# Kernel tuning notes

Measured on AMD Instinct MI355X. Metric: run time of the kernel, lower is better.

Reference implementation:

```python
import jax, jax.numpy as jnp
import numpy as np

# ---- module geometry ----
BULK = 64          # bulk (J2) integration points, 3 comps each
COH = 32           # cohesive integration points, 2 comps each
LS = BULK * 3 + COH * 2  # = 256, material layer width

# ---- J2 plasticity material constants (plane-stress, linear isotropic hardening) ----
E_MOD = 200.0
NU = 0.3
SY0 = 2.0
HARD = 10.0
G_MOD = E_MOD / (2.0 * (1.0 + NU))
_c = E_MOD / (1.0 - NU * NU)
C_EL = np.array([[_c, _c * NU, 0.0], [_c * NU, _c, 0.0], [0.0, 0.0, _c * (1.0 - NU) / 2.0]], dtype=np.float32)
C_INV = np.linalg.inv(C_EL).astype(np.float32)

# ---- Turon cohesive-zone constants (bilinear damage law) ----
K_PEN = 50.0       # penalty stiffness
DELTA0 = 0.1       # damage-onset effective jump
DELTAF = 1.0       # full-failure effective jump


def j2_update(eps, epsp, epbar):
    # eps, epsp: [B,P,3]; epbar: [B,P]. Radial-return with linear hardening.
    sig_tr = jnp.einsum('bpi,ji->bpj', eps - epsp, jnp.asarray(C_EL))
    s1, s2, s12 = sig_tr[..., 0], sig_tr[..., 1], sig_tr[..., 2]
    seq = jnp.sqrt(jnp.maximum(s1 * s1 - s1 * s2 + s2 * s2 + 3.0 * s12 * s12, 1e-12))
    f = seq - (SY0 + HARD * epbar)
    plastic = f > 0.0
    dep = jnp.where(plastic, f / (3.0 * G_MOD + HARD), 0.0)
    r = (SY0 + HARD * (epbar + dep)) / seq
    sig = jnp.where(plastic[..., None], r[..., None] * sig_tr, sig_tr)
    epsp_new = jnp.where(plastic[..., None], eps - jnp.einsum('bpj,ij->bpi', sig, jnp.asarray(C_INV)), epsp)
    return sig, epsp_new, epbar + dep


def coh_update(jump, hist):
    # jump: [B,P,2] (normal, shear); hist: [B,P] max effective jump (damage history).
    dn, ds = jump[..., 0], jump[..., 1]
    lam = jnp.sqrt(jnp.maximum(jnp.maximum(dn, 0.0) ** 2 + ds * ds, 1e-12))
    hist_new = jnp.maximum(hist, lam)
    dmg = jnp.clip(DELTAF * (hist_new - DELTA0) / (jnp.maximum(hist_new, 1e-12) * (DELTAF - DELTA0)), 0.0, 1.0)
    tn = K_PEN * dn * jnp.where(dn > 0.0, 1.0 - dmg, 1.0)  # compression is undamaged
    ts = (1.0 - dmg) * K_PEN * ds
    return jnp.stack([tn, ts], axis=-1), hist_new


def setup_inputs() -> dict:
    key = jax.random.key(0)
    k1, k2, k3 = jax.random.split(key, 3)
    x = jax.random.normal(k1, (256, 1024, 16), dtype=jnp.float32)
    W1 = jax.random.normal(k2, (LS, 16), dtype=jnp.float32) * 0.1
    W2 = jax.random.normal(k3, (16, LS), dtype=jnp.float32) * 0.1
    return {"x": x, "W1": W1, "W2": W2}


def reference(x, W1, W2):
    B, T, F = x.shape
    # fc1 applied to every (batch, time) slice (original loops; here one GEMM)
    h = jnp.einsum('btf,lf->btl', x, W1)  # [B,T,LS]
    h_t = jnp.transpose(h, (1, 0, 2))     # [T,B,LS] for the time scan

    epsp0 = jnp.zeros((B, BULK, 3), dtype=x.dtype)
    epbar0 = jnp.zeros((B, BULK), dtype=x.dtype)
    hist0 = jnp.zeros((B, COH), dtype=x.dtype)

    def step(carry, ht):
        epsp, epbar, hist = carry
        eps = ht[:, : BULK * 3].reshape(B, BULK, 3)
        jmp = ht[:, BULK * 3:].reshape(B, COH, 2)
        sig, epsp, epbar = j2_update(eps, epsp, epbar)   # update + commit per step
        trac, hist = coh_update(jmp, hist)
        y = jnp.concatenate([sig.reshape(B, -1), trac.reshape(B, -1)], axis=-1)
        return (epsp, epbar, hist), y

    _, ys = jax.lax.scan(step, (epsp0, epbar0, hist0), h_t)  # [T,B,LS]
    ys = jnp.transpose(ys, (1, 0, 2))  # [B,T,LS]
    # softLayer fc2: linear with softplus-constrained (non-negative) weights
    out = jnp.einsum('btl,ol->bto', ys, jax.nn.softplus(W2))
    return out
```

## Files before the change

### kernel.cpp

```cpp
#include <hip/hip_runtime.h>
#include <cmath>
#include <cstdint>

#define BATCH  256
#define TT     1024
#define FIN    16
#define LSZ    256
#define NBULK  64
#define NCOH   32
#define TC     32
#define NCHUNK (TT / TC)
#define HBS    260
#define HCS    68
#define YSS    336

typedef __attribute__((ext_vector_type(8))) short short8;
typedef __attribute__((ext_vector_type(4))) float floatx4;

__device__ __forceinline__ unsigned short f2bf_rne(float f) {
    union { float f; unsigned int i; } v; v.f = f;
    unsigned int b = v.i;
    return (unsigned short)((b + 0x7FFFu + ((b >> 16) & 1u)) >> 16);
}
__device__ __forceinline__ unsigned int bfbits(float f) {
    union { float f; unsigned int i; } v; v.f = f;
    return v.i + 0x8000u;
}
__device__ __forceinline__ float u2f(unsigned int u) {
    union { unsigned int i; float f; } v; v.i = u; return v.f;
}

#define BARRIER() asm volatile("s_waitcnt lgkmcnt(0)\n\ts_barrier" ::: "memory")

#define MC00   219.78021978021977f
#define MC01   65.93406593406593f
#define MC22   76.92307692307692f
#define MSY0   2.0f
#define AK     0.958466453674121406f
#define BK     0.041533546325878594f

__global__ __launch_bounds__(256, 1)
void fused_mat_kernel(const float* __restrict__ x,
                      const float* __restrict__ w1,
                      const float* __restrict__ w2,
                      float* __restrict__ out)
{
    __shared__ __attribute__((aligned(16))) float          s_hb[2][TC][HBS];
    __shared__ __attribute__((aligned(16))) float          s_hc[2][TC][HCS];
    __shared__ __attribute__((aligned(16))) unsigned short s_y [2][TC][YSS];

    const int tid  = threadIdx.x;
    const int b    = blockIdx.x;
    const int lane = tid & 63;
    const int wv   = tid >> 6;
    const int m    = lane & 15;
    const int q    = lane >> 4;

    const size_t xrow = (size_t)b * TT;

    short8 w1fd[12];
    short8 w1f4[4];
    short8 vf[10];
    uint4  rxc[2][2], rxp[2][2];

    if (wv == 2) {
        #pragma unroll
        for (int n = 0; n < 12; ++n) {
            #pragma unroll
            for (int j = 0; j < 8; ++j) {
                float v = 0.f;
                if (q < 2) {
                    const int l = n * 16 + m, c = l / 3, cm = l - 3 * c, f = q * 8 + j;
                    const float wa = w1[(3 * c + 0) * FIN + f];
                    const float wb = w1[(3 * c + 1) * FIN + f];
                    const float wc = w1[(3 * c + 2) * FIN + f];
                    v = (cm == 0) ? fmaf(MC01, wb, MC00 * wa)
                      : (cm == 1) ? fmaf(MC00, wb, MC01 * wa)
                                  : MC22 * wc;
                }
                w1fd[n][j] = (short)f2bf_rne(v);
            }
        }
        #pragma unroll
        for (int n = 12; n < 16; ++n) {
            #pragma unroll
            for (int j = 0; j < 8; ++j) {
                unsigned short v = 0;
                if (q < 2) v = f2bf_rne(w1[(n * 16 + m) * FIN + q * 8 + j]);
                w1f4[n - 12][j] = (short)v;
            }
        }
        #pragma unroll
        for (int mt = 0; mt < 2; ++mt) {
            short8 ax, adx;
            #pragma unroll
            for (int j = 0; j < 8; ++j) {
                float xc = 0.f, xp = 0.f;
                if (q < 2) {
                    const int rowB = mt * 16 + m;
                    xc = x[(xrow + rowB) * FIN + q * 8 + j];
                    if (rowB > 0) xp = x[(xrow + rowB - 1) * FIN + q * 8 + j];
                }
                ax[j]  = (short)f2bf_rne(xc);
                adx[j] = (short)f2bf_rne(xc - xp);
            }
            #pragma unroll
            for (int n = 0; n < 16; ++n) {
                floatx4 acc = {0.f, 0.f, 0.f, 0.f};
                acc = (n < 12)
                    ? __builtin_amdgcn_mfma_f32_16x16x32_bf16(adx, w1fd[n], acc, 0, 0, 0)
                    : __builtin_amdgcn_mfma_f32_16x16x32_bf16(ax, w1f4[n - 12], acc, 0, 0, 0);
                const int col = n * 16 + m;
                if (n < 12) {
                    const int cc = col / 3, cm = col - cc * 3;
                    #pragma unroll
                    for (int r = 0; r < 4; ++r)
                        s_hb[0][mt * 16 + q * 4 + r][cc * 4 + cm] = acc[r];
                } else {
                    #pragma unroll
                    for (int r = 0; r < 4; ++r)
                        s_hc[0][mt * 16 + q * 4 + r][col - 192] = acc[r];
                }
            }
        }
        if (q < 2) {
            #pragma unroll
            for (int mt = 0; mt < 2; ++mt) {
                const int rowB = TC + mt * 16 + m;
                const float* xc = x + (xrow + rowB) * FIN + q * 8;
                const float* xp = x + (xrow + rowB - 1) * FIN + q * 8;
                rxc[mt][0] = *(const uint4*)xc;  rxc[mt][1] = *(const uint4*)(xc + 4);
                rxp[mt][0] = *(const uint4*)xp;  rxp[mt][1] = *(const uint4*)(xp + 4);
            }
        }
    } else if (wv == 3) {
        #pragma unroll
        for (int ks = 0; ks < 10; ++ks) {
            #pragma unroll
            for (int j = 0; j < 8; ++j) {
                const int p = ks * 32 + q * 8 + j;
                unsigned short v = 0;
                if (p < 256) {
                    const int comp = p & 3;
                    if (comp < 3) {
                        const int l = 3 * (p >> 2) + comp;
                        float xv = w2[m * LSZ + l];
                        float sp = fmaxf(xv, 0.0f) + log1pf(expf(-fabsf(xv)));
                        v = f2bf_rne(sp);
                    }
                } else {
                    const int l = p - 64;
                    float xv = w2[m * LSZ + l];
                    float sp = fmaxf(xv, 0.0f) + log1pf(expf(-fabsf(xv)));
                    v = f2bf_rne(sp);
                }
                vf[ks][j] = (short)v;
            }
        }
    }

    float sg0 = 0.f, sg1 = 0.f, sg2 = 0.f, syv = MSY0;
    float hist = 0.f;

    __syncthreads();

    for (int i = 0; i <= NCHUNK; ++i) {
        if (wv == 0) {
            if (i < NCHUNK) {
                const float* hb = &s_hb[i & 1][0][0];
                unsigned short* yb = &s_y[i & 1][0][0];
                const int off = lane * 4;
                #pragma unroll
                for (int t = 0; t < TC; ++t) {
                    const floatx4 dv = *(const floatx4*)(hb + t * HBS + off);
                    const float pre = AK * syv;
                    const float t0 = sg0 + dv.x, t1 = sg1 + dv.y, t2 = sg2 + dv.z;
                    const float a1 = t0 * (t0 - t1);
                    const float b1 = fmaf(t1, t1, 3.0f * (t2 * t2));
                    const float qq = fmaxf(a1 + b1, 1e-12f);
                    const float rs  = __builtin_amdgcn_rsqf(qq);
                    const float seq = qq * rs;
                    const float rr  = fminf(fmaf(pre, rs, BK), 1.0f);
                    sg0 = rr * t0; sg1 = rr * t1; sg2 = rr * t2;
                    syv = fmaf(BK, fmaxf(seq - syv, 0.0f), syv);
                    uint2 pk;
                    pk.x = (bfbits(sg0) >> 16) | (bfbits(sg1) & 0xFFFF0000u);
                    pk.y = (bfbits(sg2) >> 16);
                    *(uint2*)(yb + t * YSS + off) = pk;
                }
            }
        } else if (wv == 1) {
            if (i < NCHUNK && lane < NCOH) {
                const float* hc = &s_hc[i & 1][0][0];
                unsigned short* yb = &s_y[i & 1][0][0];
                const int off = 2 * lane;
                #pragma unroll
                for (int t = 0; t < TC; ++t) {
                    const float2 jv = *(const float2*)(hc + t * HCS + off);
                    const float dn = jv.x, ds = jv.y;
                    const float dnp = fmaxf(dn, 0.0f);
                    const float lam = __builtin_amdgcn_sqrtf(fmaxf(fmaf(dnp, dnp, ds * ds), 1e-12f));
                    hist = fmaxf(hist, lam);
                    float dmg = (hist - 0.1f) * __builtin_amdgcn_rcpf(hist * 0.9f);
                    dmg = fminf(fmaxf(dmg, 0.0f), 1.0f);
                    const float om = 1.0f - dmg;
                    const float tn = 50.0f * dn * (dn > 0.0f ? om : 1.0f);
                    const float ts = om * 50.0f * ds;
                    unsigned int pk = (bfbits(tn) >> 16) | (bfbits(ts) & 0xFFFF0000u);
                    *(unsigned int*)(yb + t * YSS + 256 + off) = pk;
                }
            }
        } else if (wv == 2) {
            if (i + 1 < NCHUNK) {
                short8 ax[2], adx[2];
                #pragma unroll
                for (int mt = 0; mt < 2; ++mt) {
                    const unsigned int wc[8] = {rxc[mt][0].x, rxc[mt][0].y, rxc[mt][0].z, rxc[mt][0].w,
                                                rxc[mt][1].x, rxc[mt][1].y, rxc[mt][1].z, rxc[mt][1].w};
                    const unsigned int wp[8] = {rxp[mt][0].x, rxp[mt][0].y, rxp[mt][0].z, rxp[mt][0].w,
                                                rxp[mt][1].x, rxp[mt][1].y, rxp[mt][1].z, rxp[mt][1].w};
                    #pragma unroll
                    for (int j = 0; j < 8; ++j) {
                        unsigned short va = 0, vd = 0;
                        if (q < 2) {
                            const float xc = u2f(wc[j]), xp = u2f(wp[j]);
                            va = f2bf_rne(xc);
                            vd = f2bf_rne(xc - xp);
                        }
                        ax[mt][j]  = (short)va;
                        adx[mt][j] = (short)vd;
                    }
                }
                if (i + 2 < NCHUNK && q < 2) {
                    #pragma unroll
                    for (int mt = 0; mt < 2; ++mt) {
                        const int rowB = (i + 2) * TC + mt * 16 + m;
                        const float* xc = x + (xrow + rowB) * FIN + q * 8;
                        const float* xp = x + (xrow + rowB - 1) * FIN + q * 8;
                        rxc[mt][0] = *(const uint4*)xc;  rxc[mt][1] = *(const uint4*)(xc + 4);
                        rxp[mt][0] = *(const uint4*)xp;  rxp[mt][1] = *(const uint4*)(xp + 4);
                    }
                }
                float* hbw = &s_hb[(i + 1) & 1][0][0];
                float* hcw = &s_hc[(i + 1) & 1][0][0];
                #pragma unroll
                for (int mt = 0; mt < 2; ++mt) {
                    #pragma unroll
                    for (int n = 0; n < 16; ++n) {
                        floatx4 acc = {0.f, 0.f, 0.f, 0.f};
                        acc = (n < 12)
                            ? __builtin_amdgcn_mfma_f32_16x16x32_bf16(adx[mt], w1fd[n], acc, 0, 0, 0)
                            : __builtin_amdgcn_mfma_f32_16x16x32_bf16(ax[mt], w1f4[n - 12], acc, 0, 0, 0);
                        const int col = n * 16 + m;
                        if (n < 12) {
                            const int cc = col / 3, cm = col - cc * 3;
                            #pragma unroll
                            for (int r = 0; r < 4; ++r)
                                hbw[(mt * 16 + q * 4 + r) * HBS + cc * 4 + cm] = acc[r];
                        } else {
                            #pragma unroll
                            for (int r = 0; r < 4; ++r)
                                hcw[(mt * 16 + q * 4 + r) * HCS + col - 192] = acc[r];
                        }
                    }
                }
            }
        } else {
            if (i >= 1) {
                const int t0 = (i - 1) * TC;
                const unsigned short* yb = &s_y[(i - 1) & 1][0][0];
                #pragma unroll
                for (int mt = 0; mt < 2; ++mt) {
                    floatx4 a0 = {0.f, 0.f, 0.f, 0.f};
                    floatx4 a1 = {0.f, 0.f, 0.f, 0.f};
                    #pragma unroll
                    for (int ks = 0; ks < 5; ++ks) {
                        const short8* yp = (const short8*)(yb + (mt * 16 + m) * YSS + ks * 32 + q * 8);
                        a0 = __builtin_amdgcn_mfma_f32_16x16x32_bf16(*yp, vf[ks], a0, 0, 0, 0);
                    }
                    #pragma unroll
                    for (int ks = 5; ks < 10; ++ks) {
                        const short8* yp = (const short8*)(yb + (mt * 16 + m) * YSS + ks * 32 + q * 8);
                        a1 = __builtin_amdgcn_mfma_f32_16x16x32_bf16(*yp, vf[ks], a1, 0, 0, 0);
                    }
                    #pragma unroll
                    for (int r = 0; r < 4; ++r)
                        out[(xrow + t0 + mt * 16 + q * 4 + r) * FIN + m] = a0[r] + a1[r];
                }
            }
        }
        BARRIER();
    }
}

extern "C" void kernel_launch(void* const* d_in, const int* in_sizes, int n_in,
                              void* d_out, int out_size, void* d_ws, size_t ws_size,
                              hipStream_t stream) {
    const float* x  = (const float*)d_in[0];
    const float* w1 = (const float*)d_in[1];
    const float* w2 = (const float*)d_in[2];
    float* out = (float*)d_out;
    fused_mat_kernel<<<BATCH, 256, 0, stream>>>(x, w1, w2, out);
}
```

Before: 160.6 us.

## Split bulk GEMM into bf16 hi/lo terms and batch LDS loads in recurrence waves

The bulk-strain GEMM path now splits the increment inputs and the folded W1 weights into bf16 high and low parts. It issues three MFMAs per tile instead of one, which recovers near-fp32 accuracy for the accumulated stress trial. The J2 and cohesive recurrence waves now prefetch eight timesteps of LDS inputs into registers, double-buffered behind scheduling barriers, so the serial per-step chain does not wait on individual LDS loads. The cost is triple the MFMA work in the producer wave and more register pressure.

```diff
diff --git a/kernel.cpp b/kernel.cpp
--- a/kernel.cpp
+++ b/kernel.cpp
@@ -29,6 +29,11 @@
 __device__ __forceinline__ float u2f(unsigned int u) {
     union { unsigned int i; float f; } v; v.i = u; return v.f;
 }
+__device__ __forceinline__ void bfsplit(float v, unsigned short& hi, unsigned short& lo) {
+    unsigned short h = f2bf_rne(v);
+    lo = f2bf_rne(v - u2f((unsigned int)h << 16));
+    hi = h;
+}
 
 #define BARRIER() asm volatile("s_waitcnt lgkmcnt(0)\n\ts_barrier" ::: "memory")
 
@@ -58,7 +63,7 @@
 
     const size_t xrow = (size_t)b * TT;
 
-    short8 w1fd[12];
+    short8 w1fdh[12], w1fdl[12];
     short8 w1f4[4];
     short8 vf[10];
     uint4  rxc[2][2], rxp[2][2];
@@ -78,7 +83,10 @@
                       : (cm == 1) ? fmaf(MC00, wb, MC01 * wa)
                                   : MC22 * wc;
                 }
-                w1fd[n][j] = (short)f2bf_rne(v);
+                unsigned short hi, lo;
+                bfsplit(v, hi, lo);
+                w1fdh[n][j] = (short)hi;
+                w1fdl[n][j] = (short)lo;
             }
         }
         #pragma unroll
@@ -92,7 +100,7 @@
         }
         #pragma unroll
         for (int mt = 0; mt < 2; ++mt) {
-            short8 ax, adx;
+            short8 ax, adh, adl;
             #pragma unroll
             for (int j = 0; j < 8; ++j) {
                 float xc = 0.f, xp = 0.f;
@@ -101,15 +109,22 @@
                     xc = x[(xrow + rowB) * FIN + q * 8 + j];
                     if (rowB > 0) xp = x[(xrow + rowB - 1) * FIN + q * 8 + j];
                 }
+                unsigned short hi, lo;
+                bfsplit(xc - xp, hi, lo);
                 ax[j]  = (short)f2bf_rne(xc);
-                adx[j] = (short)f2bf_rne(xc - xp);
+                adh[j] = (short)hi;
+                adl[j] = (short)lo;
             }
             #pragma unroll
             for (int n = 0; n < 16; ++n) {
                 floatx4 acc = {0.f, 0.f, 0.f, 0.f};
-                acc = (n < 12)
-                    ? __builtin_amdgcn_mfma_f32_16x16x32_bf16(adx, w1fd[n], acc, 0, 0, 0)
-                    : __builtin_amdgcn_mfma_f32_16x16x32_bf16(ax, w1f4[n - 12], acc, 0, 0, 0);
+                if (n < 12) {
+                    acc = __builtin_amdgcn_mfma_f32_16x16x32_bf16(adh, w1fdh[n], acc, 0, 0, 0);
+                    acc = __builtin_amdgcn_mfma_f32_16x16x32_bf16(adl, w1fdh[n], acc, 0, 0, 0);
+                    acc = __builtin_amdgcn_mfma_f32_16x16x32_bf16(adh, w1fdl[n], acc, 0, 0, 0);
+                } else {
+                    acc = __builtin_amdgcn_mfma_f32_16x16x32_bf16(ax, w1f4[n - 12], acc, 0, 0, 0);
+                }
                 const int col = n * 16 + m;
                 if (n < 12) {
                     const int cc = col / 3, cm = col - cc * 3;
@@ -170,23 +185,39 @@
                 const float* hb = &s_hb[i & 1][0][0];
                 unsigned short* yb = &s_y[i & 1][0][0];
                 const int off = lane * 4;
-                #pragma unroll
-                for (int t = 0; t < TC; ++t) {
-                    const floatx4 dv = *(const floatx4*)(hb + t * HBS + off);
-                    const float pre = AK * syv;
-                    const float t0 = sg0 + dv.x, t1 = sg1 + dv.y, t2 = sg2 + dv.z;
-                    const float a1 = t0 * (t0 - t1);
-                    const float b1 = fmaf(t1, t1, 3.0f * (t2 * t2));
-                    const float qq = fmaxf(a1 + b1, 1e-12f);
-                    const float rs  = __builtin_amdgcn_rsqf(qq);
-                    const float seq = qq * rs;
-                    const float rr  = fminf(fmaf(pre, rs, BK), 1.0f);
-                    sg0 = rr * t0; sg1 = rr * t1; sg2 = rr * t2;
-                    syv = fmaf(BK, fmaxf(seq - syv, 0.0f), syv);
-                    uint2 pk;
-                    pk.x = (bfbits(sg0) >> 16) | (bfbits(sg1) & 0xFFFF0000u);
-                    pk.y = (bfbits(sg2) >> 16);
-                    *(uint2*)(yb + t * YSS + off) = pk;
+                floatx4 ev[2][8];
+                #pragma unroll
+                for (int t = 0; t < 8; ++t)
+                    ev[0][t] = *(const floatx4*)(hb + t * HBS + off);
+                __builtin_amdgcn_sched_barrier(0);
+                #pragma unroll
+                for (int g = 0; g < 4; ++g) {
+                    if (g + 1 < 4) {
+                        #pragma unroll
+                        for (int t = 0; t < 8; ++t)
+                            ev[(g + 1) & 1][t] =
+                                *(const floatx4*)(hb + ((g + 1) * 8 + t) * HBS + off);
+                        __builtin_amdgcn_sched_barrier(0);
+                    }
+                    #pragma unroll
+                    for (int tt = 0; tt < 8; ++tt) {
+                        const int t = g * 8 + tt;
+                        const floatx4 dv = ev[g & 1][tt];
+                        const float pre = AK * syv;
+                        const float t0 = sg0 + dv.x, t1 = sg1 + dv.y, t2 = sg2 + dv.z;
+                        const float a1 = t0 * (t0 - t1);
+                        const float b1 = fmaf(t1, t1, 3.0f * (t2 * t2));
+                        const float qq = fmaxf(a1 + b1, 1e-12f);
+                        const float rs  = __builtin_amdgcn_rsqf(qq);
+                        const float seq = qq * rs;
+                        const float rr  = fminf(fmaf(pre, rs, BK), 1.0f);
+                        sg0 = rr * t0; sg1 = rr * t1; sg2 = rr * t2;
+                        syv = fmaf(BK, fmaxf(seq - syv, 0.0f), syv);
+                        uint2 pk;
+                        pk.x = (bfbits(sg0) >> 16) | (bfbits(sg1) & 0xFFFF0000u);
+                        pk.y = (bfbits(sg2) >> 16);
+                        *(uint2*)(yb + t * YSS + off) = pk;
+                    }
                 }
             }
         } else if (wv == 1) {
@@ -194,25 +225,40 @@
                 const float* hc = &s_hc[i & 1][0][0];
                 unsigned short* yb = &s_y[i & 1][0][0];
                 const int off = 2 * lane;
-                #pragma unroll
-                for (int t = 0; t < TC; ++t) {
-                    const float2 jv = *(const float2*)(hc + t * HCS + off);
-                    const float dn = jv.x, ds = jv.y;
-                    const float dnp = fmaxf(dn, 0.0f);
-                    const float lam = __builtin_amdgcn_sqrtf(fmaxf(fmaf(dnp, dnp, ds * ds), 1e-12f));
-                    hist = fmaxf(hist, lam);
-                    float dmg = (hist - 0.1f) * __builtin_amdgcn_rcpf(hist * 0.9f);
-                    dmg = fminf(fmaxf(dmg, 0.0f), 1.0f);
-                    const float om = 1.0f - dmg;
-                    const float tn = 50.0f * dn * (dn > 0.0f ? om : 1.0f);
-                    const float ts = om * 50.0f * ds;
-                    unsigned int pk = (bfbits(tn) >> 16) | (bfbits(ts) & 0xFFFF0000u);
-                    *(unsigned int*)(yb + t * YSS + 256 + off) = pk;
+                float2 jv[2][8];
+                #pragma unroll
+                for (int t = 0; t < 8; ++t)
+                    jv[0][t] = *(const float2*)(hc + t * HCS + off);
+                __builtin_amdgcn_sched_barrier(0);
+                #pragma unroll
+                for (int g = 0; g < 4; ++g) {
+                    if (g + 1 < 4) {
+                        #pragma unroll
+                        for (int t = 0; t < 8; ++t)
+                            jv[(g + 1) & 1][t] =
+                                *(const float2*)(hc + ((g + 1) * 8 + t) * HCS + off);
+                        __builtin_amdgcn_sched_barrier(0);
+                    }
+                    #pragma unroll
+                    for (int tt = 0; tt < 8; ++tt) {
+                        const int t = g * 8 + tt;
+                        const float dn = jv[g & 1][tt].x, ds = jv[g & 1][tt].y;
+                        const float dnp = fmaxf(dn, 0.0f);
+                        const float lam = __builtin_amdgcn_sqrtf(fmaxf(fmaf(dnp, dnp, ds * ds), 1e-12f));
+                        hist = fmaxf(hist, lam);
+                        float dmg = (hist - 0.1f) * __builtin_amdgcn_rcpf(hist * 0.9f);
+                        dmg = fminf(fmaxf(dmg, 0.0f), 1.0f);
+                        const float om = 1.0f - dmg;
+                        const float tn = 50.0f * dn * (dn > 0.0f ? om : 1.0f);
+                        const float ts = om * 50.0f * ds;
+                        unsigned int pk = (bfbits(tn) >> 16) | (bfbits(ts) & 0xFFFF0000u);
+                        *(unsigned int*)(yb + t * YSS + 256 + off) = pk;
+                    }
                 }
             }
         } else if (wv == 2) {
             if (i + 1 < NCHUNK) {
-                short8 ax[2], adx[2];
+                short8 ax[2], adh[2], adl[2];
                 #pragma unroll
                 for (int mt = 0; mt < 2; ++mt) {
                     const unsigned int wc[8] = {rxc[mt][0].x, rxc[mt][0].y, rxc[mt][0].z, rxc[mt][0].w,
@@ -221,14 +267,15 @@
                                                 rxp[mt][1].x, rxp[mt][1].y, rxp[mt][1].z, rxp[mt][1].w};
                     #pragma unroll
                     for (int j = 0; j < 8; ++j) {
-                        unsigned short va = 0, vd = 0;
+                        unsigned short va = 0, vh = 0, vl = 0;
                         if (q < 2) {
                             const float xc = u2f(wc[j]), xp = u2f(wp[j]);
                             va = f2bf_rne(xc);
-                            vd = f2bf_rne(xc - xp);
+                            bfsplit(xc - xp, vh, vl);
                         }
                         ax[mt][j]  = (short)va;
-                        adx[mt][j] = (short)vd;
+                        adh[mt][j] = (short)vh;
+                        adl[mt][j] = (short)vl;
                     }
                 }
                 if (i + 2 < NCHUNK && q < 2) {
@@ -248,9 +295,13 @@
                     #pragma unroll
                     for (int n = 0; n < 16; ++n) {
                         floatx4 acc = {0.f, 0.f, 0.f, 0.f};
-                        acc = (n < 12)
-                            ? __builtin_amdgcn_mfma_f32_16x16x32_bf16(adx[mt], w1fd[n], acc, 0, 0, 0)
-                            : __builtin_amdgcn_mfma_f32_16x16x32_bf16(ax[mt], w1f4[n - 12], acc, 0, 0, 0);
+                        if (n < 12) {
+                            acc = __builtin_amdgcn_mfma_f32_16x16x32_bf16(adh[mt], w1fdh[n], acc, 0, 0, 0);
+                            acc = __builtin_amdgcn_mfma_f32_16x16x32_bf16(adl[mt], w1fdh[n], acc, 0, 0, 0);
+                            acc = __builtin_amdgcn_mfma_f32_16x16x32_bf16(adh[mt], w1fdl[n], acc, 0, 0, 0);
+                        } else {
+                            acc = __builtin_amdgcn_mfma_f32_16x16x32_bf16(ax[mt], w1f4[n - 12], acc, 0, 0, 0);
+                        }
                         const int col = n * 16 + m;
                         if (n < 12) {
                             const int cc = col / 3, cm = col - cc * 3;
```

Measured after the change: 163.3 us. Within noise of the previous version (+1.7%).

## Rotate J2 stress basis, split-bf16 fc1, halve chunk size, move bf16 packing to fc2

Applied to the files above, without the earlier changes.

Rewrites the J2 recurrence in a rotated (u,v,w) stress basis so the equivalent-stress form is diagonal. The basis change and the cohesive penalty scale are folded into the W1 and softplus(W2) fragments. The fc1 bulk GEMM now uses a hi/lo bf16 split (three MFMAs) for better accuracy. The time chunk shrinks from 32 to 16 steps, which shortens the pipeline fill and drain but doubles the number of barriers. Material outputs are stored to LDS as fp32, and the fc2 wave converts them to bf16, taking packing work off the serial recurrence waves at the cost of more LDS traffic.

```diff
diff --git a/kernel.cpp b/kernel.cpp
--- a/kernel.cpp
+++ b/kernel.cpp
@@ -6,13 +6,12 @@
 #define TT     1024
 #define FIN    16
 #define LSZ    256
-#define NBULK  64
 #define NCOH   32
-#define TC     32
+#define TC     16
 #define NCHUNK (TT / TC)
 #define HBS    260
 #define HCS    68
-#define YSS    336
+#define YFS    324
 
 typedef __attribute__((ext_vector_type(8))) short short8;
 typedef __attribute__((ext_vector_type(4))) float floatx4;
@@ -22,18 +21,23 @@
     unsigned int b = v.i;
     return (unsigned short)((b + 0x7FFFu + ((b >> 16) & 1u)) >> 16);
 }
-__device__ __forceinline__ unsigned int bfbits(float f) {
+__device__ __forceinline__ unsigned short f2bf_hu(float f) {
     union { float f; unsigned int i; } v; v.f = f;
-    return v.i + 0x8000u;
+    return (unsigned short)((v.i + 0x8000u) >> 16);
 }
 __device__ __forceinline__ float u2f(unsigned int u) {
     union { unsigned int i; float f; } v; v.i = u; return v.f;
 }
+__device__ __forceinline__ void bfsplit(float v, unsigned short& hi, unsigned short& lo) {
+    unsigned short h = f2bf_rne(v);
+    lo = f2bf_rne(v - u2f((unsigned int)h << 16));
+    hi = h;
+}
 
 #define BARRIER() asm volatile("s_waitcnt lgkmcnt(0)\n\ts_barrier" ::: "memory")
 
-#define MC00   219.78021978021977f
-#define MC01   65.93406593406593f
+#define MCU    285.71428571428571f
+#define MCV    153.84615384615384f
 #define MC22   76.92307692307692f
 #define MSY0   2.0f
 #define AK     0.958466453674121406f
@@ -45,9 +49,9 @@
                       const float* __restrict__ w2,
                       float* __restrict__ out)
 {
-    __shared__ __attribute__((aligned(16))) float          s_hb[2][TC][HBS];
-    __shared__ __attribute__((aligned(16))) float          s_hc[2][TC][HCS];
-    __shared__ __attribute__((aligned(16))) unsigned short s_y [2][TC][YSS];
+    __shared__ __attribute__((aligned(16))) float s_hb[2][TC][HBS];
+    __shared__ __attribute__((aligned(16))) float s_hc[2][TC][HCS];
+    __shared__ __attribute__((aligned(16))) float s_yf[2][TC][YFS];
 
     const int tid  = threadIdx.x;
     const int b    = blockIdx.x;
@@ -58,10 +62,10 @@
 
     const size_t xrow = (size_t)b * TT;
 
-    short8 w1fd[12];
+    short8 w1fdh[12], w1fdl[12];
     short8 w1f4[4];
     short8 vf[10];
-    uint4  rxc[2][2], rxp[2][2];
+    uint4  rxc[2], rxp[2];
 
     if (wv == 2) {
         #pragma unroll
@@ -74,11 +78,14 @@
                     const float wa = w1[(3 * c + 0) * FIN + f];
                     const float wb = w1[(3 * c + 1) * FIN + f];
                     const float wc = w1[(3 * c + 2) * FIN + f];
-                    v = (cm == 0) ? fmaf(MC01, wb, MC00 * wa)
-                      : (cm == 1) ? fmaf(MC00, wb, MC01 * wa)
+                    v = (cm == 0) ? MCU * (wa + wb)
+                      : (cm == 1) ? MCV * (wa - wb)
                                   : MC22 * wc;
                 }
-                w1fd[n][j] = (short)f2bf_rne(v);
+                unsigned short hi, lo;
+                bfsplit(v, hi, lo);
+                w1fdh[n][j] = (short)hi;
+                w1fdl[n][j] = (short)lo;
             }
         }
         #pragma unroll
@@ -90,48 +97,50 @@
                 w1f4[n - 12][j] = (short)v;
             }
         }
-        #pragma unroll
-        for (int mt = 0; mt < 2; ++mt) {
-            short8 ax, adx;
+        {
+            short8 ax, adh, adl;
             #pragma unroll
             for (int j = 0; j < 8; ++j) {
                 float xc = 0.f, xp = 0.f;
                 if (q < 2) {
-                    const int rowB = mt * 16 + m;
-                    xc = x[(xrow + rowB) * FIN + q * 8 + j];
-                    if (rowB > 0) xp = x[(xrow + rowB - 1) * FIN + q * 8 + j];
-                }
+                    xc = x[(xrow + m) * FIN + q * 8 + j];
+                    if (m > 0) xp = x[(xrow + m - 1) * FIN + q * 8 + j];
+                }
+                unsigned short hi, lo;
+                bfsplit(xc - xp, hi, lo);
                 ax[j]  = (short)f2bf_rne(xc);
-                adx[j] = (short)f2bf_rne(xc - xp);
+                adh[j] = (short)hi;
+                adl[j] = (short)lo;
             }
             #pragma unroll
             for (int n = 0; n < 16; ++n) {
                 floatx4 acc = {0.f, 0.f, 0.f, 0.f};
-                acc = (n < 12)
-                    ? __builtin_amdgcn_mfma_f32_16x16x32_bf16(adx, w1fd[n], acc, 0, 0, 0)
-                    : __builtin_amdgcn_mfma_f32_16x16x32_bf16(ax, w1f4[n - 12], acc, 0, 0, 0);
+                if (n < 12) {
+                    acc = __builtin_amdgcn_mfma_f32_16x16x32_bf16(adh, w1fdh[n], acc, 0, 0, 0);
+                    acc = __builtin_amdgcn_mfma_f32_16x16x32_bf16(adl, w1fdh[n], acc, 0, 0, 0);
+                    acc = __builtin_amdgcn_mfma_f32_16x16x32_bf16(adh, w1fdl[n], acc, 0, 0, 0);
+                } else {
+                    acc = __builtin_amdgcn_mfma_f32_16x16x32_bf16(ax, w1f4[n - 12], acc, 0, 0, 0);
+                }
                 const int col = n * 16 + m;
                 if (n < 12) {
                     const int cc = col / 3, cm = col - cc * 3;
                     #pragma unroll
                     for (int r = 0; r < 4; ++r)
-                        s_hb[0][mt * 16 + q * 4 + r][cc * 4 + cm] = acc[r];
+                        s_hb[0][q * 4 + r][cc * 4 + cm] = acc[r];
                 } else {
                     #pragma unroll
                     for (int r = 0; r < 4; ++r)
-                        s_hc[0][mt * 16 + q * 4 + r][col - 192] = acc[r];
+                        s_hc[0][q * 4 + r][col - 192] = acc[r];
                 }
             }
         }
         if (q < 2) {
-            #pragma unroll
-            for (int mt = 0; mt < 2; ++mt) {
-                const int rowB = TC + mt * 16 + m;
-                const float* xc = x + (xrow + rowB) * FIN + q * 8;
-                const float* xp = x + (xrow + rowB - 1) * FIN + q * 8;
-                rxc[mt][0] = *(const uint4*)xc;  rxc[mt][1] = *(const uint4*)(xc + 4);
-                rxp[mt][0] = *(const uint4*)xp;  rxp[mt][1] = *(const uint4*)(xp + 4);
-            }
+            const int rowB = TC + m;
+            const float* xc = x + (xrow + rowB) * FIN + q * 8;
+            const float* xp = x + (xrow + rowB - 1) * FIN + q * 8;
+            rxc[0] = *(const uint4*)xc;  rxc[1] = *(const uint4*)(xc + 4);
+            rxp[0] = *(const uint4*)xp;  rxp[1] = *(const uint4*)(xp + 4);
         }
     } else if (wv == 3) {
         #pragma unroll
@@ -139,27 +148,31 @@
             #pragma unroll
             for (int j = 0; j < 8; ++j) {
                 const int p = ks * 32 + q * 8 + j;
-                unsigned short v = 0;
+                float v = 0.f;
                 if (p < 256) {
                     const int comp = p & 3;
                     if (comp < 3) {
-                        const int l = 3 * (p >> 2) + comp;
-                        float xv = w2[m * LSZ + l];
-                        float sp = fmaxf(xv, 0.0f) + log1pf(expf(-fabsf(xv)));
-                        v = f2bf_rne(sp);
+                        const int c = p >> 2;
+                        const float w0v = w2[m * LSZ + 3 * c + 0];
+                        const float w1v = w2[m * LSZ + 3 * c + 1];
+                        const float w2v = w2[m * LSZ + 3 * c + 2];
+                        const float sp0 = fmaxf(w0v, 0.f) + log1pf(expf(-fabsf(w0v)));
+                        const float sp1 = fmaxf(w1v, 0.f) + log1pf(expf(-fabsf(w1v)));
+                        const float sp2 = fmaxf(w2v, 0.f) + log1pf(expf(-fabsf(w2v)));
+                        v = (comp == 0) ? 0.5f * (sp0 + sp1)
+                          : (comp == 1) ? 0.5f * (sp0 - sp1)
+                                        : sp2;
                     }
                 } else {
-                    const int l = p - 64;
-                    float xv = w2[m * LSZ + l];
-                    float sp = fmaxf(xv, 0.0f) + log1pf(expf(-fabsf(xv)));
-                    v = f2bf_rne(sp);
-                }
-                vf[ks][j] = (short)v;
+                    const float xv = w2[m * LSZ + (p - 64)];
+                    v = 50.0f * (fmaxf(xv, 0.f) + log1pf(expf(-fabsf(xv))));
+                }
+                vf[ks][j] = (short)f2bf_rne(v);
             }
         }
     }
 
-    float sg0 = 0.f, sg1 = 0.f, sg2 = 0.f, syv = MSY0;
+    float sgu = 0.f, sgv = 0.f, sgw = 0.f, syv = MSY0;
     float hist = 0.f;
 
     __syncthreads();
@@ -168,125 +181,128 @@
         if (wv == 0) {
             if (i < NCHUNK) {
                 const float* hb = &s_hb[i & 1][0][0];
-                unsigned short* yb = &s_y[i & 1][0][0];
+                float* yb = &s_yf[i & 1][0][0];
                 const int off = lane * 4;
+                floatx4 ev[TC];
+                #pragma unroll
+                for (int t = 0; t < TC; ++t)
+                    ev[t] = *(const floatx4*)(hb + t * HBS + off);
                 #pragma unroll
                 for (int t = 0; t < TC; ++t) {
-                    const floatx4 dv = *(const floatx4*)(hb + t * HBS + off);
-                    const float pre = AK * syv;
-                    const float t0 = sg0 + dv.x, t1 = sg1 + dv.y, t2 = sg2 + dv.z;
-                    const float a1 = t0 * (t0 - t1);
-                    const float b1 = fmaf(t1, t1, 3.0f * (t2 * t2));
-                    const float qq = fmaxf(a1 + b1, 1e-12f);
+                    const float u = sgu + ev[t].x;
+                    const float v = sgv + ev[t].y;
+                    const float w = sgw + ev[t].z;
+                    const float qq = fmaxf(
+                        fmaf(0.25f * u, u, fmaf(0.75f * v, v, (3.0f * w) * w)), 1e-12f);
                     const float rs  = __builtin_amdgcn_rsqf(qq);
                     const float seq = qq * rs;
+                    const float pre = AK * syv;
                     const float rr  = fminf(fmaf(pre, rs, BK), 1.0f);
-                    sg0 = rr * t0; sg1 = rr * t1; sg2 = rr * t2;
-                    syv = fmaf(BK, fmaxf(seq - syv, 0.0f), syv);
-                    uint2 pk;
-                    pk.x = (bfbits(sg0) >> 16) | (bfbits(sg1) & 0xFFFF0000u);
-                    pk.y = (bfbits(sg2) >> 16);
-                    *(uint2*)(yb + t * YSS + off) = pk;
+                    sgu = rr * u; sgv = rr * v; sgw = rr * w;
+                    syv = fmaxf(syv, fmaf(BK, seq, pre));
+                    floatx4 st = {sgu, sgv, sgw, 0.0f};
+                    *(floatx4*)(yb + t * YFS + off) = st;
                 }
             }
         } else if (wv == 1) {
             if (i < NCHUNK && lane < NCOH) {
                 const float* hc = &s_hc[i & 1][0][0];
-                unsigned short* yb = &s_y[i & 1][0][0];
+                float* yb = &s_yf[i & 1][0][0];
                 const int off = 2 * lane;
+                float2 jv[TC];
+                #pragma unroll
+                for (int t = 0; t < TC; ++t)
+                    jv[t] = *(const float2*)(hc + t * HCS + off);
                 #pragma unroll
                 for (int t = 0; t < TC; ++t) {
-                    const float2 jv = *(const float2*)(hc + t * HCS + off);
-                    const float dn = jv.x, ds = jv.y;
+                    const float dn = jv[t].x, ds = jv[t].y;
                     const float dnp = fmaxf(dn, 0.0f);
                     const float lam = __builtin_amdgcn_sqrtf(fmaxf(fmaf(dnp, dnp, ds * ds), 1e-12f));
                     hist = fmaxf(hist, lam);
                     float dmg = (hist - 0.1f) * __builtin_amdgcn_rcpf(hist * 0.9f);
                     dmg = fminf(fmaxf(dmg, 0.0f), 1.0f);
                     const float om = 1.0f - dmg;
-                    const float tn = 50.0f * dn * (dn > 0.0f ? om : 1.0f);
-                    const float ts = om * 50.0f * ds;
-                    unsigned int pk = (bfbits(tn) >> 16) | (bfbits(ts) & 0xFFFF0000u);
-                    *(unsigned int*)(yb + t * YSS + 256 + off) = pk;
+                    float2 st;
+                    st.x = dn * (dn > 0.0f ? om : 1.0f);
+                    st.y = om * ds;
+                    *(float2*)(yb + t * YFS + 256 + off) = st;
                 }
             }
         } else if (wv == 2) {
             if (i + 1 < NCHUNK) {
-                short8 ax[2], adx[2];
-                #pragma unroll
-                for (int mt = 0; mt < 2; ++mt) {
-                    const unsigned int wc[8] = {rxc[mt][0].x, rxc[mt][0].y, rxc[mt][0].z, rxc[mt][0].w,
-                                                rxc[mt][1].x, rxc[mt][1].y, rxc[mt][1].z, rxc[mt][1].w};
-                    const unsigned int wp[8] = {rxp[mt][0].x, rxp[mt][0].y, rxp[mt][0].z, rxp[mt][0].w,
-                                                rxp[mt][1].x, rxp[mt][1].y, rxp[mt][1].z, rxp[mt][1].w};
+                short8 ax, adh, adl;
+                {
+                    const unsigned int wc[8] = {rxc[0].x, rxc[0].y, rxc[0].z, rxc[0].w,
+                                                rxc[1].x, rxc[1].y, rxc[1].z, rxc[1].w};
+                    const unsigned int wp[8] = {rxp[0].x, rxp[0].y, rxp[0].z, rxp[0].w,
+                                                rxp[1].x, rxp[1].y, rxp[1].z, rxp[1].w};
                     #pragma unroll
                     for (int j = 0; j < 8; ++j) {
-                        unsigned short va = 0, vd = 0;
+                        unsigned short va = 0, vh = 0, vl = 0;
                         if (q < 2) {
                             const float xc = u2f(wc[j]), xp = u2f(wp[j]);
                             va = f2bf_rne(xc);
-                            vd = f2bf_rne(xc - xp);
+                            bfsplit(xc - xp, vh, vl);
                         }
-                        ax[mt][j]  = (short)va;
-                        adx[mt][j] = (short)vd;
+                        ax[j]  = (short)va;
+                        adh[j] = (short)vh;
+                        adl[j] = (short)vl;
                     }
                 }
                 if (i + 2 < NCHUNK && q < 2) {
-                    #pragma unroll
-                    for (int mt = 0; mt < 2; ++mt) {
-                        const int rowB = (i + 2) * TC + mt * 16 + m;
-                        const float* xc = x + (xrow + rowB) * FIN + q * 8;
-                        const float* xp = x + (xrow + rowB - 1) * FIN + q * 8;
-                        rxc[mt][0] = *(const uint4*)xc;  rxc[mt][1] = *(const uint4*)(xc + 4);
-                        rxp[mt][0] = *(const uint4*)xp;  rxp[mt][1] = *(const uint4*)(xp + 4);
-                    }
+                    const int rowB = (i + 2) * TC + m;
+                    const float* xc = x + (xrow + rowB) * FIN + q * 8;
+                    const float* xp = x + (xrow + rowB - 1) * FIN + q * 8;
+                    rxc[0] = *(const uint4*)xc;  rxc[1] = *(const uint4*)(xc + 4);
+                    rxp[0] = *(const uint4*)xp;  rxp[1] = *(const uint4*)(xp + 4);
                 }
                 float* hbw = &s_hb[(i + 1) & 1][0][0];
                 float* hcw = &s_hc[(i + 1) & 1][0][0];
                 #pragma unroll
-                for (int mt = 0; mt < 2; ++mt) {
-                    #pragma unroll
-                    for (int n = 0; n < 16; ++n) {
-                        floatx4 acc = {0.f, 0.f, 0.f, 0.f};
-                        acc = (n < 12)
-                            ? __builtin_amdgcn_mfma_f32_16x16x32_bf16(adx[mt], w1fd[n], acc, 0, 0, 0)
-                            : __builtin_amdgcn_mfma_f32_16x16x32_bf16(ax[mt], w1f4[n - 12], acc, 0, 0, 0);
-                        const int col = n * 16 + m;
-                        if (n < 12) {
-                            const int cc = col / 3, cm = col - cc * 3;
-                            #pragma unroll
-                            for (int r = 0; r < 4; ++r)
-                                hbw[(mt * 16 + q * 4 + r) * HBS + cc * 4 + cm] = acc[r];
-                        } else {
-                            #pragma unroll
-                            for (int r = 0; r < 4; ++r)
-                                hcw[(mt * 16 + q * 4 + r) * HCS + col - 192] = acc[r];
-                        }
+                for (int n = 0; n < 16; ++n) {
+                    floatx4 acc = {0.f, 0.f, 0.f, 0.f};
+                    if (n < 12) {
+                        acc = __builtin_amdgcn_mfma_f32_16x16x32_bf16(adh, w1fdh[n], acc, 0, 0, 0);
+                        acc = __builtin_amdgcn_mfma_f32_16x16x32_bf16(adl, w1fdh[n], acc, 0, 0, 0);
+                        acc = __builtin_amdgcn_mfma_f32_16x16x32_bf16(adh, w1fdl[n], acc, 0, 0, 0);
+                    } else {
+                        acc = __builtin_amdgcn_mfma_f32_16x16x32_bf16(ax, w1f4[n - 12], acc, 0, 0, 0);
+                    }
+                    const int col = n * 16 + m;
+                    if (n < 12) {
+                        const int cc = col / 3, cm = col - cc * 3;
+                        #pragma unroll
+                        for (int r = 0; r < 4; ++r)
+                            hbw[(q * 4 + r) * HBS + cc * 4 + cm] = acc[r];
+                    } else {
+                        #pragma unroll
+                        for (int r = 0; r < 4; ++r)
+                            hcw[(q * 4 + r) * HCS + col - 192] = acc[r];
                     }
                 }
             }
         } else {
             if (i >= 1) {
                 const int t0 = (i - 1) * TC;
-                const unsigned short* yb = &s_y[(i - 1) & 1][0][0];
-                #pragma unroll
-                for (int mt = 0; mt < 2; ++mt) {
-                    floatx4 a0 = {0.f, 0.f, 0.f, 0.f};
-                    floatx4 a1 = {0.f, 0.f, 0.f, 0.f};
-                    #pragma unroll
-                    for (int ks = 0; ks < 5; ++ks) {
-                        const short8* yp = (const short8*)(yb + (mt * 16 + m) * YSS + ks * 32 + q * 8);
-                        a0 = __builtin_amdgcn_mfma_f32_16x16x32_bf16(*yp, vf[ks], a0, 0, 0, 0);
-                    }
-                    #pragma unroll
-                    for (int ks = 5; ks < 10; ++ks) {
-                        const short8* yp = (const short8*)(yb + (mt * 16 + m) * YSS + ks * 32 + q * 8);
-                        a1 = __builtin_amdgcn_mfma_f32_16x16x32_bf16(*yp, vf[ks], a1, 0, 0, 0);
-                    }
-                    #pragma unroll
-                    for (int r = 0; r < 4; ++r)
-                        out[(xrow + t0 + mt * 16 + q * 4 + r) * FIN + m] = a0[r] + a1[r];
-                }
+                const float* yb = &s_yf[(i - 1) & 1][0][0];
+                floatx4 a0 = {0.f, 0.f, 0.f, 0.f};
+                floatx4 a1 = {0.f, 0.f, 0.f, 0.f};
+                #pragma unroll
+                for (int ks = 0; ks < 10; ++ks) {
+                    const float* yp = yb + m * YFS + ks * 32 + q * 8;
+                    const floatx4 f0 = *(const floatx4*)yp;
+                    const floatx4 f1 = *(const floatx4*)(yp + 4);
+                    short8 yf;
+                    yf[0] = (short)f2bf_hu(f0.x); yf[1] = (short)f2bf_hu(f0.y);
+                    yf[2] = (short)f2bf_hu(f0.z); yf[3] = (short)f2bf_hu(f0.w);
+                    yf[4] = (short)f2bf_hu(f1.x); yf[5] = (short)f2bf_hu(f1.y);
+                    yf[6] = (short)f2bf_hu(f1.z); yf[7] = (short)f2bf_hu(f1.w);
+                    if (ks < 5) a0 = __builtin_amdgcn_mfma_f32_16x16x32_bf16(yf, vf[ks], a0, 0, 0, 0);
+                    else        a1 = __builtin_amdgcn_mfma_f32_16x16x32_bf16(yf, vf[ks], a1, 0, 0, 0);
+                }
+                #pragma unroll
+                for (int r = 0; r < 4; ++r)
+                    out[(xrow + t0 + q * 4 + r) * FIN + m] = a0[r] + a1[r];
             }
         }
         BARRIER();
```

After: 168.9 us. +5.2%, slower.
